# Optimization experiments

Measured on AMD Instinct MI355X. Metric: run time of the kernel, lower is better.

Reference implementation:

```python
import jax, jax.numpy as jnp
import numpy as np

BITS = 4
GROUP = 128
MAXQ = 2 ** BITS - 1  # 15 for asymmetric 4-bit


def round_ste(x):
    # straight-through rounding: round in fwd, identity in bwd
    return x + jax.lax.stop_gradient(jnp.round(x) - x)


def quant_weight(weight, v, min_scale, max_scale):
    """Groupwise asymmetric fake-quant (quantize + dequantize) of weight.

    weight: [O, I], v: [O, I] learnable rounding offsets,
    min_scale/max_scale: [O*I/GROUP] learnable min/max scales in [-1, 0].
    """
    O, I = weight.shape
    w = weight.reshape(-1, GROUP)          # [G, GROUP]
    vv = v.reshape(-1, GROUP)              # [G, GROUP]
    wmin_t = jnp.minimum(w.min(axis=1), 0.0)  # [G]
    wmax_t = jnp.maximum(w.max(axis=1), 0.0)  # [G]
    # forward clamps min/max scale into [-1, 0] before use
    wmin = wmin_t * (jnp.clip(min_scale, -1.0, 0.0) + 1.0)
    wmax = wmax_t * (jnp.clip(max_scale, -1.0, 0.0) + 1.0)
    degenerate = (wmin == 0.0) & (wmax == 0.0)
    wmin = jnp.where(degenerate, -1.0, wmin)
    wmax = jnp.where(degenerate, 1.0, wmax)
    # scale stored at fp16 precision (scale_dtype), then used in fp32 math
    scale = ((wmax - wmin) / MAXQ).astype(jnp.float16).astype(weight.dtype)  # [G]
    zp = round_ste(-wmin / scale)                                            # [G]
    int_w = round_ste(w / scale[:, None] + vv)                               # [G, GROUP]
    q = jnp.clip(int_w + zp[:, None], 0.0, float(MAXQ))
    wq = scale[:, None] * (q - zp[:, None])
    return wq.reshape(O, I)


def setup_inputs() -> dict:
    key = jax.random.key(0)
    k_x, k_w, k_b, k_v = jax.random.split(key, 4)
    O, I = 4096, 4096
    B, S = 2, 2048
    x = jax.random.normal(k_x, (B, S, I), dtype=jnp.float32)
    weight = jax.random.normal(k_w, (O, I), dtype=jnp.float32) * 0.02
    bias = jax.random.normal(k_b, (O,), dtype=jnp.float32) * 0.02
    value = jax.random.normal(k_v, (O, I), dtype=jnp.float32) * 0.1
    n_groups = O * I // GROUP
    min_scale = jnp.zeros((n_groups,), dtype=jnp.float32)
    max_scale = jnp.zeros((n_groups,), dtype=jnp.float32)
    return {"x": x, "weight": weight, "bias": bias, "value": value,
            "min_scale": min_scale, "max_scale": max_scale}


def reference(x, weight, bias, value, min_scale, max_scale):
    wq = quant_weight(weight, value, min_scale, max_scale)  # [O, I]
    # F.linear(x, weight_q, bias): x @ wq.T + bias
    return jnp.einsum('bsi,oi->bso', x, wq) + bias
```

## Files before the change

kernel.cpp:

```cpp
#include <hip/hip_runtime.h>
#include <hip/hip_bf16.h>
#include <hip/hip_fp16.h>
#include <stdint.h>

#define M_DIM 4096
#define N_DIM 4096
#define K_DIM 4096
#define GROUPSZ 128
#define MAXQ 15.0f

#define BM 256
#define BN 256
#define BK 64
#define T_TILES (K_DIM / BK)

#define QUANT_BLOCKS (N_DIM * K_DIM / GROUPSZ / 4)
#define CAST_BLOCKS  (M_DIM * K_DIM / (256 * 8))

typedef __attribute__((ext_vector_type(8))) short short8;
typedef __attribute__((ext_vector_type(4))) float f32x4;

__global__ __launch_bounds__(256) void prep_kernel(
    const float* __restrict__ weight, const float* __restrict__ value,
    const float* __restrict__ min_scale, const float* __restrict__ max_scale,
    __hip_bfloat16* __restrict__ wq,
    const float* __restrict__ x, __hip_bfloat16* __restrict__ xb)
{
    const int bidx = blockIdx.x;
    const int tid  = threadIdx.x;
    if (bidx < QUANT_BLOCKS) {
        const int wave = tid >> 6;
        const int lane = tid & 63;
        const long g    = (long)bidx * 4 + wave;
        const long base = g * GROUPSZ + lane * 2;

        const float2 w = *(const float2*)(weight + base);
        const float2 v = *(const float2*)(value  + base);

        float mn = fminf(w.x, w.y);
        float mx = fmaxf(w.x, w.y);
#pragma unroll
        for (int off = 32; off >= 1; off >>= 1) {
            mn = fminf(mn, __shfl_xor(mn, off, 64));
            mx = fmaxf(mx, __shfl_xor(mx, off, 64));
        }
        mn = fminf(mn, 0.0f);
        mx = fmaxf(mx, 0.0f);

        const float ms = fminf(fmaxf(min_scale[g], -1.0f), 0.0f) + 1.0f;
        const float xs = fminf(fmaxf(max_scale[g], -1.0f), 0.0f) + 1.0f;
        float wmin = mn * ms;
        float wmax = mx * xs;
        if (wmin == 0.0f && wmax == 0.0f) { wmin = -1.0f; wmax = 1.0f; }

        const float scale = (float)(_Float16)((wmax - wmin) / MAXQ);
        const float zp    = rintf(-wmin / scale);

        const float q0 = fminf(fmaxf(rintf(w.x / scale + v.x) + zp, 0.0f), MAXQ);
        const float q1 = fminf(fmaxf(rintf(w.y / scale + v.y) + zp, 0.0f), MAXQ);
        const float o0 = scale * (q0 - zp);
        const float o1 = scale * (q1 - zp);

        __hip_bfloat162 o;
        o.x = __float2bfloat16(o0);
        o.y = __float2bfloat16(o1);
        *(__hip_bfloat162*)(wq + base) = o;
    } else {
        const long i = ((long)(bidx - QUANT_BLOCKS) * 256 + tid) * 8;
        const float4 a = *(const float4*)(x + i);
        const float4 b = *(const float4*)(x + i + 4);
        union { short8 s; __hip_bfloat16 h[8]; } u;
        u.h[0] = __float2bfloat16(a.x);
        u.h[1] = __float2bfloat16(a.y);
        u.h[2] = __float2bfloat16(a.z);
        u.h[3] = __float2bfloat16(a.w);
        u.h[4] = __float2bfloat16(b.x);
        u.h[5] = __float2bfloat16(b.y);
        u.h[6] = __float2bfloat16(b.z);
        u.h[7] = __float2bfloat16(b.w);
        *(short8*)(xb + i) = u.s;
    }
}

__global__ __launch_bounds__(512, 2) void gemm_kernel(
    const __hip_bfloat16* __restrict__ A,
    const __hip_bfloat16* __restrict__ B,
    const float* __restrict__ bias,
    float* __restrict__ C)
{
    __shared__ __align__(16) char lds[131072];

    const int tid  = threadIdx.x;
    const int lane = tid & 63;
    const int wv   = tid >> 6;
    const int wm   = wv >> 2;
    const int wn   = wv & 3;

    const int bid = blockIdx.x;
    const int swz = (bid & 7) * (gridDim.x >> 3) + (bid >> 3);
    const int brow = (swz >> 4) * BM;
    const int bcol = (swz & 15) * BN;

    const int stg_r = tid >> 3;
    const int cc    = ((tid & 7) ^ (stg_r & 7)) * 8;

#define STAGE(XP, rowbase, h, tau, ldsbase)                                         \
    { _Pragma("unroll")                                                             \
      for (int inst = 0; inst < 2; ++inst) {                                        \
        const __hip_bfloat16* g = (XP) +                                            \
            (size_t)((rowbase) + (h) * 128 + inst * 64 + stg_r) * K_DIM +           \
            (tau) * 64 + cc;                                                        \
        __builtin_amdgcn_global_load_lds(                                           \
            (const __attribute__((address_space(1))) void*)g,                       \
            (__attribute__((address_space(3))) void*)(lds + (ldsbase) +             \
                (h) * 16384 + inst * 8192 + (wv << 10)),                            \
            16, 0, 0);                                                              \
      } }

    const int ro = lane & 15;
    const int hi = lane >> 4;
    const int slot0 = ((0 + hi) ^ (ro & 7)) << 4;
    const int slot1 = ((4 + hi) ^ (ro & 7)) << 4;
    const int rbA = (wm * 128 + ro) * 128;
    const int rbB = (wn * 64  + ro) * 128;

    f32x4 acc[8][4] = {};

#define MFMA_C(M0, AF, BF)                                                          \
    { _Pragma("unroll")                                                             \
      for (int n = 0; n < 4; ++n) {                                                 \
        _Pragma("unroll")                                                           \
        for (int mm = 0; mm < 4; ++mm)                                              \
            acc[(M0) + mm][n] = __builtin_amdgcn_mfma_f32_16x16x32_bf16(            \
                AF[mm], BF[n], acc[(M0) + mm][n], 0, 0, 0);                         \
      } }

#define RDA4(dst, base, M0, S)                                                      \
    dst[0] = *(const short8*)((base) + ((M0) + 0) * 2048 + (S));                    \
    dst[1] = *(const short8*)((base) + ((M0) + 1) * 2048 + (S));                    \
    dst[2] = *(const short8*)((base) + ((M0) + 2) * 2048 + (S));                    \
    dst[3] = *(const short8*)((base) + ((M0) + 3) * 2048 + (S));

#define RDB4(dst, base, S)                                                          \
    dst[0] = *(const short8*)((base) + 0 * 2048 + (S));                             \
    dst[1] = *(const short8*)((base) + 1 * 2048 + (S));                             \
    dst[2] = *(const short8*)((base) + 2 * 2048 + (S));                             \
    dst[3] = *(const short8*)((base) + 3 * 2048 + (S));

    short8 bfr0[4], bfr1[4];
    short8 afA[4], afB[4], afC[4], afD[4];

    STAGE(A, brow, 0, 0, 0);
    STAGE(A, brow, 1, 0, 0);
    STAGE(B, bcol, 0, 0, 65536);
    STAGE(B, bcol, 1, 0, 65536);
    asm volatile("s_waitcnt vmcnt(0)" ::: "memory");
    __builtin_amdgcn_s_barrier();
    RDA4(afA, lds + rbA, 0, slot0);
    RDB4(bfr0, lds + 65536 + rbB, slot0);

#pragma unroll 1
    for (int t = 0; t < T_TILES; ++t) {
        const int c = t & 1;
        const char* bA  = lds + c * 32768 + rbA;
        const char* bB  = lds + 65536 + c * 32768 + rbB;
        const char* bAn = lds + (c ^ 1) * 32768 + rbA;
        const char* bBn = lds + 65536 + (c ^ 1) * 32768 + rbB;

        if (t + 1 < T_TILES) {
            STAGE(A, brow, 0, t + 1, (c ^ 1) * 32768);
            STAGE(A, brow, 1, t + 1, (c ^ 1) * 32768);
        }

        RDA4(afB, bA, 4, slot0);
        RDB4(bfr1, bB, slot1);
        asm volatile("s_waitcnt lgkmcnt(8)" ::: "memory");
        __builtin_amdgcn_sched_barrier(0);
        __builtin_amdgcn_s_setprio(1);
        MFMA_C(0, afA, bfr0);
        __builtin_amdgcn_s_setprio(0);
        if (t + 1 < T_TILES) { STAGE(B, bcol, 0, t + 1, 65536 + (c ^ 1) * 32768); }

        RDA4(afC, bA, 0, slot1);
        asm volatile("s_waitcnt lgkmcnt(8)" ::: "memory");
        __builtin_amdgcn_sched_barrier(0);
        __builtin_amdgcn_s_setprio(1);
        MFMA_C(4, afB, bfr0);
        __builtin_amdgcn_s_setprio(0);
        if (t + 1 < T_TILES) { STAGE(B, bcol, 1, t + 1, 65536 + (c ^ 1) * 32768); }

        RDA4(afD, bA, 4, slot1);
        asm volatile("s_waitcnt lgkmcnt(4)" ::: "memory");
        __builtin_amdgcn_sched_barrier(0);
        __builtin_amdgcn_s_setprio(1);
        MFMA_C(0, afC, bfr1);
        __builtin_amdgcn_s_setprio(0);

        asm volatile("s_waitcnt lgkmcnt(0)" ::: "memory");
        __builtin_amdgcn_sched_barrier(0);

        if (t + 1 < T_TILES) {
            asm volatile("s_waitcnt vmcnt(0)" ::: "memory");
            __builtin_amdgcn_s_barrier();
            RDA4(afA, bAn, 0, slot0);
            RDB4(bfr0, bBn, slot0);
            __builtin_amdgcn_sched_barrier(0);
        }

        __builtin_amdgcn_s_setprio(1);
        MFMA_C(4, afD, bfr1);
        __builtin_amdgcn_s_setprio(0);
    }

    const int col   = lane & 15;
    const int rbase = hi * 4;
    float bv[4];
#pragma unroll
    for (int n = 0; n < 4; ++n)
        bv[n] = bias[bcol + wn * 64 + n * 16 + col];

#pragma unroll
    for (int m = 0; m < 8; ++m) {
        const int mrow = brow + wm * 128 + m * 16 + rbase;
#pragma unroll
        for (int r = 0; r < 4; ++r) {
            float* crow = C + (size_t)(mrow + r) * N_DIM + bcol + wn * 64 + col;
#pragma unroll
            for (int n = 0; n < 4; ++n)
                crow[n * 16] = acc[m][n][r] + bv[n];
        }
    }
#undef STAGE
#undef MFMA_C
#undef RDA4
#undef RDB4
}

extern "C" void kernel_launch(void* const* d_in, const int* in_sizes, int n_in,
                              void* d_out, int out_size, void* d_ws, size_t ws_size,
                              hipStream_t stream) {
    const float* x         = (const float*)d_in[0];
    const float* weight    = (const float*)d_in[1];
    const float* bias      = (const float*)d_in[2];
    const float* value     = (const float*)d_in[3];
    const float* min_scale = (const float*)d_in[4];
    const float* max_scale = (const float*)d_in[5];
    float* out = (float*)d_out;

    __hip_bfloat16* xb  = (__hip_bfloat16*)d_ws;
    __hip_bfloat16* wqb = xb + (size_t)M_DIM * K_DIM;

    prep_kernel<<<QUANT_BLOCKS + CAST_BLOCKS, 256, 0, stream>>>(
        weight, value, min_scale, max_scale, wqb, x, xb);
    gemm_kernel<<<(M_DIM / BM) * (N_DIM / BN), 512, 0, stream>>>(xb, wqb, bias, out);
}
```

Before: 166.4 us.

## Load B fragments directly from global into registers, halve LDS

The B operand no longer goes through LDS. Each wave loads its B MFMA fragments straight from global memory into registers, double-buffered across a 2x unrolled tile loop, and LDS shrinks to 64KB for the A tiles only. This removes LDS staging traffic and the matching ds_reads for B, and the lower LDS footprint could allow more occupancy. In exchange, B loads are no longer shared between the waves in a block, so each wave issues its own global loads with less coalescing, and the vmcnt wait accounting becomes more fragile.

```diff
diff --git a/kernel.cpp b/kernel.cpp
--- a/kernel.cpp
+++ b/kernel.cpp
@@ -88,7 +88,7 @@
     const float* __restrict__ bias,
     float* __restrict__ C)
 {
-    __shared__ __align__(16) char lds[131072];
+    __shared__ __align__(16) char lds[65536];
 
     const int tid  = threadIdx.x;
     const int lane = tid & 63;
@@ -104,25 +104,34 @@
     const int stg_r = tid >> 3;
     const int cc    = ((tid & 7) ^ (stg_r & 7)) * 8;
 
-#define STAGE(XP, rowbase, h, tau, ldsbase)                                         \
+#define STAGE_A(tau, bc)                                                            \
     { _Pragma("unroll")                                                             \
-      for (int inst = 0; inst < 2; ++inst) {                                        \
-        const __hip_bfloat16* g = (XP) +                                            \
-            (size_t)((rowbase) + (h) * 128 + inst * 64 + stg_r) * K_DIM +           \
-            (tau) * 64 + cc;                                                        \
-        __builtin_amdgcn_global_load_lds(                                           \
-            (const __attribute__((address_space(1))) void*)g,                       \
-            (__attribute__((address_space(3))) void*)(lds + (ldsbase) +             \
-                (h) * 16384 + inst * 8192 + (wv << 10)),                            \
-            16, 0, 0);                                                              \
-      } }
+      for (int h = 0; h < 2; ++h)                                                   \
+        _Pragma("unroll")                                                           \
+        for (int inst = 0; inst < 2; ++inst) {                                      \
+            const __hip_bfloat16* g = A +                                           \
+                (size_t)(brow + h * 128 + inst * 64 + stg_r) * K_DIM +              \
+                (tau) * 64 + cc;                                                    \
+            __builtin_amdgcn_global_load_lds(                                       \
+                (const __attribute__((address_space(1))) void*)g,                   \
+                (__attribute__((address_space(3))) void*)(lds + (bc) * 32768 +      \
+                    h * 16384 + inst * 8192 + (wv << 10)),                          \
+                16, 0, 0);                                                          \
+        } }
 
     const int ro = lane & 15;
     const int hi = lane >> 4;
     const int slot0 = ((0 + hi) ^ (ro & 7)) << 4;
     const int slot1 = ((4 + hi) ^ (ro & 7)) << 4;
     const int rbA = (wm * 128 + ro) * 128;
-    const int rbB = (wn * 64  + ro) * 128;
+
+    const __hip_bfloat16* pB = B + (size_t)(bcol + wn * 64 + ro) * K_DIM + hi * 8;
+
+#define LDB(dst, t_, kk)                                                            \
+    dst[0] = *(const short8*)(pB + 0 * 16 * K_DIM + (t_) * 64 + (kk) * 32);         \
+    dst[1] = *(const short8*)(pB + 1 * 16 * K_DIM + (t_) * 64 + (kk) * 32);         \
+    dst[2] = *(const short8*)(pB + 2 * 16 * K_DIM + (t_) * 64 + (kk) * 32);         \
+    dst[3] = *(const short8*)(pB + 3 * 16 * K_DIM + (t_) * 64 + (kk) * 32);
 
     f32x4 acc[8][4] = {};
 
@@ -141,75 +150,70 @@
     dst[2] = *(const short8*)((base) + ((M0) + 2) * 2048 + (S));                    \
     dst[3] = *(const short8*)((base) + ((M0) + 3) * 2048 + (S));
 
-#define RDB4(dst, base, S)                                                          \
-    dst[0] = *(const short8*)((base) + 0 * 2048 + (S));                             \
-    dst[1] = *(const short8*)((base) + 1 * 2048 + (S));                             \
-    dst[2] = *(const short8*)((base) + 2 * 2048 + (S));                             \
-    dst[3] = *(const short8*)((base) + 3 * 2048 + (S));
-
-    short8 bfr0[4], bfr1[4];
+    short8 Bk0a[4], Bk1a[4], Bk0b[4], Bk1b[4];
     short8 afA[4], afB[4], afC[4], afD[4];
 
-    STAGE(A, brow, 0, 0, 0);
-    STAGE(A, brow, 1, 0, 0);
-    STAGE(B, bcol, 0, 0, 65536);
-    STAGE(B, bcol, 1, 0, 65536);
+    STAGE_A(0, 0);
+    LDB(Bk0a, 0, 0);
+    LDB(Bk1a, 0, 1);
     asm volatile("s_waitcnt vmcnt(0)" ::: "memory");
     __builtin_amdgcn_s_barrier();
     RDA4(afA, lds + rbA, 0, slot0);
-    RDB4(bfr0, lds + 65536 + rbB, slot0);
+
+#define TILE(T_, BK0, BK1, BN0, BN1)                                                \
+    {                                                                               \
+        const int t_ = (T_);                                                        \
+        const int c_ = t_ & 1;                                                      \
+        const char* bA  = lds + c_ * 32768 + rbA;                                   \
+        const char* bAn = lds + (c_ ^ 1) * 32768 + rbA;                             \
+        asm volatile("s_waitcnt vmcnt(4)" ::: "memory");             \
+        __builtin_amdgcn_sched_barrier(0);                                          \
+        if (t_ + 1 < T_TILES) {                                                     \
+            STAGE_A(t_ + 1, c_ ^ 1);                                                \
+            LDB(BN0, t_ + 1, 0);                                                    \
+        }                                                                           \
+                                                                            \
+        RDA4(afB, bA, 4, slot0);                                                    \
+        asm volatile("s_waitcnt lgkmcnt(4)" ::: "memory");           \
+        __builtin_amdgcn_sched_barrier(0);                                          \
+        __builtin_amdgcn_s_setprio(1);                                              \
+        MFMA_C(0, afA, BK0);                                                        \
+        __builtin_amdgcn_s_setprio(0);                                              \
+                                                                            \
+        RDA4(afC, bA, 0, slot1);                                                    \
+        asm volatile("s_waitcnt lgkmcnt(4)" ::: "memory");           \
+        __builtin_amdgcn_sched_barrier(0);                                          \
+        __builtin_amdgcn_s_setprio(1);                                              \
+        MFMA_C(4, afB, BK0);                                                        \
+        __builtin_amdgcn_s_setprio(0);                                              \
+                                                                            \
+        RDA4(afD, bA, 4, slot1);                                                    \
+        asm volatile("s_waitcnt lgkmcnt(4)" ::: "memory");           \
+        if (t_ + 1 < T_TILES) { asm volatile("s_waitcnt vmcnt(8)" ::: "memory"); }  \
+        else                  { asm volatile("s_waitcnt vmcnt(0)" ::: "memory"); }  \
+        __builtin_amdgcn_sched_barrier(0);                                          \
+        __builtin_amdgcn_s_setprio(1);                                              \
+        MFMA_C(0, afC, BK1);                                                        \
+        __builtin_amdgcn_s_setprio(0);                                              \
+        if (t_ + 1 < T_TILES) { LDB(BN1, t_ + 1, 1); }                              \
+                                                                          \
+        asm volatile("s_waitcnt lgkmcnt(0)" ::: "memory");           \
+        __builtin_amdgcn_sched_barrier(0);                                          \
+        if (t_ + 1 < T_TILES) {                                                     \
+            asm volatile("s_waitcnt vmcnt(8)" ::: "memory");      \
+            __builtin_amdgcn_s_barrier();                                           \
+            RDA4(afA, bAn, 0, slot0);                                               \
+            __builtin_amdgcn_sched_barrier(0);                                      \
+        }                                                                           \
+        __builtin_amdgcn_s_setprio(1);                                              \
+        MFMA_C(4, afD, BK1);                                                        \
+        __builtin_amdgcn_s_setprio(0);                                              \
+    }
 
 #pragma unroll 1
-    for (int t = 0; t < T_TILES; ++t) {
-        const int c = t & 1;
-        const char* bA  = lds + c * 32768 + rbA;
-        const char* bB  = lds + 65536 + c * 32768 + rbB;
-        const char* bAn = lds + (c ^ 1) * 32768 + rbA;
-        const char* bBn = lds + 65536 + (c ^ 1) * 32768 + rbB;
-
-        if (t + 1 < T_TILES) {
-            STAGE(A, brow, 0, t + 1, (c ^ 1) * 32768);
-            STAGE(A, brow, 1, t + 1, (c ^ 1) * 32768);
-        }
-
-        RDA4(afB, bA, 4, slot0);
-        RDB4(bfr1, bB, slot1);
-        asm volatile("s_waitcnt lgkmcnt(8)" ::: "memory");
-        __builtin_amdgcn_sched_barrier(0);
-        __builtin_amdgcn_s_setprio(1);
-        MFMA_C(0, afA, bfr0);
-        __builtin_amdgcn_s_setprio(0);
-        if (t + 1 < T_TILES) { STAGE(B, bcol, 0, t + 1, 65536 + (c ^ 1) * 32768); }
-
-        RDA4(afC, bA, 0, slot1);
-        asm volatile("s_waitcnt lgkmcnt(8)" ::: "memory");
-        __builtin_amdgcn_sched_barrier(0);
-        __builtin_amdgcn_s_setprio(1);
-        MFMA_C(4, afB, bfr0);
-        __builtin_amdgcn_s_setprio(0);
-        if (t + 1 < T_TILES) { STAGE(B, bcol, 1, t + 1, 65536 + (c ^ 1) * 32768); }
-
-        RDA4(afD, bA, 4, slot1);
-        asm volatile("s_waitcnt lgkmcnt(4)" ::: "memory");
-        __builtin_amdgcn_sched_barrier(0);
-        __builtin_amdgcn_s_setprio(1);
-        MFMA_C(0, afC, bfr1);
-        __builtin_amdgcn_s_setprio(0);
-
-        asm volatile("s_waitcnt lgkmcnt(0)" ::: "memory");
-        __builtin_amdgcn_sched_barrier(0);
-
-        if (t + 1 < T_TILES) {
-            asm volatile("s_waitcnt vmcnt(0)" ::: "memory");
-            __builtin_amdgcn_s_barrier();
-            RDA4(afA, bAn, 0, slot0);
-            RDB4(bfr0, bBn, slot0);
-            __builtin_amdgcn_sched_barrier(0);
-        }
-
-        __builtin_amdgcn_s_setprio(1);
-        MFMA_C(4, afD, bfr1);
-        __builtin_amdgcn_s_setprio(0);
+    for (int tt = 0; tt < T_TILES; tt += 2) {
+        TILE(tt,     Bk0a, Bk1a, Bk0b, Bk1b);
+        TILE(tt + 1, Bk0b, Bk1b, Bk0a, Bk1a);
     }
 
     const int col   = lane & 15;
@@ -230,10 +234,11 @@
                 crow[n * 16] = acc[m][n][r] + bv[n];
         }
     }
-#undef STAGE
+#undef STAGE_A
+#undef LDB
 #undef MFMA_C
 #undef RDA4
-#undef RDB4
+#undef TILE
 }
 
 extern "C" void kernel_launch(void* const* d_in, const int* in_sizes, int n_in,
```

Measured after the change: 489.3 us. +194.0%, slower.

## Load B fragments directly from global into registers, skipping LDS staging

Applied to the files above, without the earlier changes.

The B operand is now read by each wave straight from global memory into MFMA fragment registers, one tile ahead. Only the A operand is staged through LDS, which halves the shared-memory allocation and removes the B LDS reads. The vmcnt waits are reworked to track the mixed LDS-DMA and register loads. The cost is that B is no longer shared through LDS, so global and L2 traffic for B rises because each wm half of the block loads it separately. Register pressure also goes up and the global load latency is exposed.

```diff
diff --git a/kernel.cpp b/kernel.cpp
--- a/kernel.cpp
+++ b/kernel.cpp
@@ -88,7 +88,7 @@
     const float* __restrict__ bias,
     float* __restrict__ C)
 {
-    __shared__ __align__(16) char lds[131072];
+    __shared__ __align__(16) char lds[65536];
 
     const int tid  = threadIdx.x;
     const int lane = tid & 63;
@@ -104,25 +104,34 @@
     const int stg_r = tid >> 3;
     const int cc    = ((tid & 7) ^ (stg_r & 7)) * 8;
 
-#define STAGE(XP, rowbase, h, tau, ldsbase)                                         \
+#define STAGE_A(tau, bc)                                                            \
     { _Pragma("unroll")                                                             \
-      for (int inst = 0; inst < 2; ++inst) {                                        \
-        const __hip_bfloat16* g = (XP) +                                            \
-            (size_t)((rowbase) + (h) * 128 + inst * 64 + stg_r) * K_DIM +           \
-            (tau) * 64 + cc;                                                        \
-        __builtin_amdgcn_global_load_lds(                                           \
-            (const __attribute__((address_space(1))) void*)g,                       \
-            (__attribute__((address_space(3))) void*)(lds + (ldsbase) +             \
-                (h) * 16384 + inst * 8192 + (wv << 10)),                            \
-            16, 0, 0);                                                              \
-      } }
+      for (int h = 0; h < 2; ++h)                                                   \
+        _Pragma("unroll")                                                           \
+        for (int inst = 0; inst < 2; ++inst) {                                      \
+            const __hip_bfloat16* g = A +                                           \
+                (size_t)(brow + h * 128 + inst * 64 + stg_r) * K_DIM +              \
+                (tau) * 64 + cc;                                                    \
+            __builtin_amdgcn_global_load_lds(                                       \
+                (const __attribute__((address_space(1))) void*)g,                   \
+                (__attribute__((address_space(3))) void*)(lds + (bc) * 32768 +      \
+                    h * 16384 + inst * 8192 + (wv << 10)),                          \
+                16, 0, 0);                                                          \
+        } }
 
     const int ro = lane & 15;
     const int hi = lane >> 4;
     const int slot0 = ((0 + hi) ^ (ro & 7)) << 4;
     const int slot1 = ((4 + hi) ^ (ro & 7)) << 4;
     const int rbA = (wm * 128 + ro) * 128;
-    const int rbB = (wn * 64  + ro) * 128;
+
+    const __hip_bfloat16* pB = B + (size_t)(bcol + wn * 64 + ro) * K_DIM + hi * 8;
+
+#define LDB(dst, t_, kk)                                                            \
+    dst[0] = *(const short8*)(pB + (size_t)0 * 16 * K_DIM + (t_) * 64 + (kk) * 32); \
+    dst[1] = *(const short8*)(pB + (size_t)1 * 16 * K_DIM + (t_) * 64 + (kk) * 32); \
+    dst[2] = *(const short8*)(pB + (size_t)2 * 16 * K_DIM + (t_) * 64 + (kk) * 32); \
+    dst[3] = *(const short8*)(pB + (size_t)3 * 16 * K_DIM + (t_) * 64 + (kk) * 32);
 
     f32x4 acc[8][4] = {};
 
@@ -141,56 +150,46 @@
     dst[2] = *(const short8*)((base) + ((M0) + 2) * 2048 + (S));                    \
     dst[3] = *(const short8*)((base) + ((M0) + 3) * 2048 + (S));
 
-#define RDB4(dst, base, S)                                                          \
-    dst[0] = *(const short8*)((base) + 0 * 2048 + (S));                             \
-    dst[1] = *(const short8*)((base) + 1 * 2048 + (S));                             \
-    dst[2] = *(const short8*)((base) + 2 * 2048 + (S));                             \
-    dst[3] = *(const short8*)((base) + 3 * 2048 + (S));
-
     short8 bfr0[4], bfr1[4];
     short8 afA[4], afB[4], afC[4], afD[4];
 
-    STAGE(A, brow, 0, 0, 0);
-    STAGE(A, brow, 1, 0, 0);
-    STAGE(B, bcol, 0, 0, 65536);
-    STAGE(B, bcol, 1, 0, 65536);
+    STAGE_A(0, 0);
+    LDB(bfr0, 0, 0);
+    LDB(bfr1, 0, 1);
     asm volatile("s_waitcnt vmcnt(0)" ::: "memory");
     __builtin_amdgcn_s_barrier();
     RDA4(afA, lds + rbA, 0, slot0);
-    RDB4(bfr0, lds + 65536 + rbB, slot0);
 
 #pragma unroll 1
     for (int t = 0; t < T_TILES; ++t) {
         const int c = t & 1;
         const char* bA  = lds + c * 32768 + rbA;
-        const char* bB  = lds + 65536 + c * 32768 + rbB;
         const char* bAn = lds + (c ^ 1) * 32768 + rbA;
-        const char* bBn = lds + 65536 + (c ^ 1) * 32768 + rbB;
-
-        if (t + 1 < T_TILES) {
-            STAGE(A, brow, 0, t + 1, (c ^ 1) * 32768);
-            STAGE(A, brow, 1, t + 1, (c ^ 1) * 32768);
-        }
+        const bool has1 = (t + 1 < T_TILES);
+
+        if (has1) { STAGE_A(t + 1, c ^ 1); }
 
         RDA4(afB, bA, 4, slot0);
-        RDB4(bfr1, bB, slot1);
-        asm volatile("s_waitcnt lgkmcnt(8)" ::: "memory");
+        asm volatile("s_waitcnt lgkmcnt(4)" ::: "memory");
+        if (has1) { asm volatile("s_waitcnt vmcnt(8)" ::: "memory"); }
+        else      { asm volatile("s_waitcnt vmcnt(4)" ::: "memory"); }
         __builtin_amdgcn_sched_barrier(0);
         __builtin_amdgcn_s_setprio(1);
         MFMA_C(0, afA, bfr0);
         __builtin_amdgcn_s_setprio(0);
-        if (t + 1 < T_TILES) { STAGE(B, bcol, 0, t + 1, 65536 + (c ^ 1) * 32768); }
 
         RDA4(afC, bA, 0, slot1);
-        asm volatile("s_waitcnt lgkmcnt(8)" ::: "memory");
+        asm volatile("s_waitcnt lgkmcnt(4)" ::: "memory");
         __builtin_amdgcn_sched_barrier(0);
         __builtin_amdgcn_s_setprio(1);
         MFMA_C(4, afB, bfr0);
         __builtin_amdgcn_s_setprio(0);
-        if (t + 1 < T_TILES) { STAGE(B, bcol, 1, t + 1, 65536 + (c ^ 1) * 32768); }
+        if (has1) { LDB(bfr0, t + 1, 0); }
 
         RDA4(afD, bA, 4, slot1);
         asm volatile("s_waitcnt lgkmcnt(4)" ::: "memory");
+        if (has1) { asm volatile("s_waitcnt vmcnt(8)" ::: "memory"); }
+        else      { asm volatile("s_waitcnt vmcnt(0)" ::: "memory"); }
         __builtin_amdgcn_sched_barrier(0);
         __builtin_amdgcn_s_setprio(1);
         MFMA_C(0, afC, bfr1);
@@ -198,18 +197,17 @@
 
         asm volatile("s_waitcnt lgkmcnt(0)" ::: "memory");
         __builtin_amdgcn_sched_barrier(0);
-
-        if (t + 1 < T_TILES) {
-            asm volatile("s_waitcnt vmcnt(0)" ::: "memory");
+        if (has1) {
+            asm volatile("s_waitcnt vmcnt(4)" ::: "memory");
             __builtin_amdgcn_s_barrier();
             RDA4(afA, bAn, 0, slot0);
-            RDB4(bfr0, bBn, slot0);
             __builtin_amdgcn_sched_barrier(0);
         }
 
         __builtin_amdgcn_s_setprio(1);
         MFMA_C(4, afD, bfr1);
         __builtin_amdgcn_s_setprio(0);
+        if (has1) { LDB(bfr1, t + 1, 1); }
     }
 
     const int col   = lane & 15;
@@ -230,10 +228,10 @@
                 crow[n * 16] = acc[m][n][r] + bv[n];
         }
     }
-#undef STAGE
+#undef STAGE_A
+#undef LDB
 #undef MFMA_C
 #undef RDA4
-#undef RDB4
 }
 
 extern "C" void kernel_launch(void* const* d_in, const int* in_sizes, int n_in,
```

After: 199.4 us. 1.2x slower.
